# Performance work log

Measured on AMD Instinct MI355X. Metric: run time of the kernel, lower is better.

The kernel has to match this reference:

```python
import jax, jax.numpy as jnp
import numpy as np

D_MODEL = 1024
N_HEADS = 16
HEAD_DIM = D_MODEL // N_HEADS


def setup_inputs() -> dict:
    key = jax.random.key(0)
    ks = jax.random.split(key, 5)
    B, T = 2, 2048
    x = jax.random.normal(ks[0], (B, T, D_MODEL), dtype=jnp.float32)
    s_in = 1.0 / np.sqrt(D_MODEL)
    W_qkv = jax.random.normal(ks[1], (D_MODEL, 3 * D_MODEL), dtype=jnp.float32) * s_in
    b_qkv = jnp.zeros((3 * D_MODEL,), dtype=jnp.float32)
    W_out = jax.random.normal(ks[2], (D_MODEL, D_MODEL), dtype=jnp.float32) * s_in
    b_out = jnp.zeros((D_MODEL,), dtype=jnp.float32)
    gamma = jnp.ones((D_MODEL,), dtype=jnp.float32)
    beta = jnp.zeros((D_MODEL,), dtype=jnp.float32)
    return {"x": x, "W_qkv": W_qkv, "b_qkv": b_qkv, "W_out": W_out,
            "b_out": b_out, "gamma": gamma, "beta": beta}


def _layernorm(x, gamma, beta, eps=1e-5):
    mu = jnp.mean(x, axis=-1, keepdims=True)
    var = jnp.var(x, axis=-1, keepdims=True)
    return (x - mu) * jax.lax.rsqrt(var + eps) * gamma + beta


def reference(x, W_qkv, b_qkv, W_out, b_out, gamma, beta):
    B, T, D = x.shape
    residual = x
    h = _layernorm(x, gamma, beta)
    qkv = h @ W_qkv + b_qkv                      # [B, T, 3D]
    qkv = qkv.reshape(B, T, 3, N_HEADS, HEAD_DIM)
    q = jnp.transpose(qkv[:, :, 0], (0, 2, 1, 3))  # [B, H, T, hd]
    k = jnp.transpose(qkv[:, :, 1], (0, 2, 1, 3))
    v = jnp.transpose(qkv[:, :, 2], (0, 2, 1, 3))
    scale = 1.0 / np.sqrt(HEAD_DIM)
    attn = jnp.einsum("bhqd,bhkd->bhqk", q, k) * scale
    attn = jax.nn.softmax(attn, axis=-1)
    out = jnp.einsum("bhqk,bhkd->bhqd", attn, v)   # [B, H, T, hd]
    out = jnp.transpose(out, (0, 2, 1, 3)).reshape(B, T, D)
    out = out @ W_out + b_out
    return residual + out
```

## Files before the change

kernel.cpp:

```cpp
#include <hip/hip_runtime.h>
#include <hip/hip_bf16.h>


#define DINL static __device__ __forceinline__

typedef __attribute__((ext_vector_type(8))) short bf16x8;
typedef __attribute__((ext_vector_type(4))) float f32x4;

DINL float fast_exp2(float x) { return __builtin_amdgcn_exp2f(x); }

DINL unsigned short f2bf(float f) {
  __hip_bfloat16 h = __float2bfloat16(f);
  unsigned short u;
  __builtin_memcpy(&u, &h, 2);
  return u;
}

DINL unsigned int cvt_pk_bf16(float lo, float hi) {
  unsigned int r;
  asm("v_cvt_pk_bf16_f32 %0, %1, %2" : "=v"(r) : "v"(lo), "v"(hi));
  return r;
}

DINL void gload_lds16(const void* g, void* l) {
  __builtin_amdgcn_global_load_lds((__attribute__((address_space(1))) void*)g,
                                   (__attribute__((address_space(3))) void*)l,
                                   16, 0, 0);
}

__global__ __launch_bounds__(256)
void prep_kernel(const float* __restrict__ x, const float* __restrict__ gamma,
                 const float* __restrict__ beta, unsigned short* __restrict__ h,
                 const float* __restrict__ Wqkv, unsigned short* __restrict__ WqkvT,
                 const float* __restrict__ Wout, unsigned short* __restrict__ WoutT) {
  __shared__ float tile[32][33];
  int bid = blockIdx.x;
  int t = threadIdx.x;

  if (bid < 4096) {
    float* red = &tile[0][0];
    int row = bid;
    float4 v = reinterpret_cast<const float4*>(x + (size_t)row * 1024)[t];
    float s  = v.x + v.y + v.z + v.w;
    float sq = v.x*v.x + v.y*v.y + v.z*v.z + v.w*v.w;
#pragma unroll
    for (int off = 1; off < 64; off <<= 1) {
      s  += __shfl_xor(s, off);
      sq += __shfl_xor(sq, off);
    }
    int wid = t >> 6;
    if ((t & 63) == 0) { red[wid] = s; red[4 + wid] = sq; }
    __syncthreads();
    s  = red[0] + red[1] + red[2] + red[3];
    sq = red[4] + red[5] + red[6] + red[7];
    float mu   = s * (1.0f / 1024.0f);
    float var  = sq * (1.0f / 1024.0f) - mu * mu;
    float rstd = rsqrtf(var + 1e-5f);
    float4 g = reinterpret_cast<const float4*>(gamma)[t];
    float4 b = reinterpret_cast<const float4*>(beta)[t];
    ushort4 o;
    o.x = f2bf((v.x - mu) * rstd * g.x + b.x);
    o.y = f2bf((v.y - mu) * rstd * g.y + b.y);
    o.z = f2bf((v.z - mu) * rstd * g.z + b.z);
    o.w = f2bf((v.w - mu) * rstd * g.w + b.w);
    reinterpret_cast<ushort4*>(h + (size_t)row * 1024)[t] = o;
  } else {
    const float* src;
    unsigned short* dst;
    int R = 1024, C, bx, by;
    if (bid < 7168) {
      src = Wqkv; dst = WqkvT; C = 3072;
      int k = bid - 4096; bx = k % 96; by = k / 96;
    } else {
      src = Wout; dst = WoutT; C = 1024;
      int k = bid - 7168; bx = k & 31; by = k >> 5;
    }
    int tx = t & 31, ty = t >> 5;
    int c0 = bx * 32, r0 = by * 32;
#pragma unroll
    for (int i = 0; i < 4; i++)
      tile[ty + i * 8][tx] = src[(size_t)(r0 + ty + i * 8) * C + c0 + tx];
    __syncthreads();
#pragma unroll
    for (int i = 0; i < 4; i++) {
      int r = ty + i * 8;
      dst[(size_t)(c0 + r) * R + r0 + tx] = f2bf(tile[tx][r]);
    }
  }
}

template <int BM, int MODE, int K>
__global__ __launch_bounds__(256, 4)
void gemm128(const unsigned short* __restrict__ A,
             const unsigned short* __restrict__ Bt,
             const float* __restrict__ bias,
             unsigned short* __restrict__ qdst, unsigned short* __restrict__ kdst,
             unsigned short* __restrict__ vTdst,
             const float* __restrict__ xres, float* __restrict__ out) {
  static_assert(BM == 128 || BM == 64, "");
  constexpr int MR = BM / 32;
  __shared__ unsigned short As[BM * 64];
  __shared__ unsigned short Bs[8192];
  int tid = threadIdx.x, wid = tid >> 6, lane = tid & 63;
  int l15 = lane & 15, l4 = lane >> 4;
  int brow, bcol;
  if (MODE == 0) {
    int lin = blockIdx.y * 24 + blockIdx.x;
    int nl  = (lin & 7) * 96 + (lin >> 3);
    bcol = (nl % 24) * 128;
    brow = (nl / 24) * BM;
  } else {
    brow = blockIdx.y * BM;
    bcol = blockIdx.x * 128;
  }
  int wr = wid >> 1, wc = wid & 1;
  f32x4 acc[MR][4] = {};

  for (int kt = 0; kt < K; kt += 64) {
    __syncthreads();
#pragma unroll
    for (int r = 0; r < MR; r++) {
      int c  = wid * (BM * 2) + r * 64;
      int cl = c + lane;
      int kb = cl / BM, row = cl % BM;
      gload_lds16(A + (size_t)(brow + row) * K + kt + kb * 8, As + c * 8);
    }
#pragma unroll
    for (int r = 0; r < 4; r++) {
      int c  = wid * 256 + r * 64;
      int cl = c + lane;
      int kb = cl >> 7, row = cl & 127;
      gload_lds16(Bt + (size_t)(bcol + row) * K + kt + kb * 8, Bs + c * 8);
    }
    __syncthreads();
#pragma unroll
    for (int ks = 0; ks < 2; ks++) {
      int kb = ks * 4 + l4;
      bf16x8 af[MR], bfr[4];
#pragma unroll
      for (int m = 0; m < MR; m++)
        af[m] = *reinterpret_cast<const bf16x8*>(As + (kb * BM + wr * (BM / 2) + m * 16 + l15) * 8);
#pragma unroll
      for (int n = 0; n < 4; n++)
        bfr[n] = *reinterpret_cast<const bf16x8*>(Bs + (kb * 128 + wc * 64 + n * 16 + l15) * 8);
#pragma unroll
      for (int m = 0; m < MR; m++)
#pragma unroll
        for (int n = 0; n < 4; n++) {
          if (MODE == 0)
            acc[m][n] = __builtin_amdgcn_mfma_f32_16x16x32_bf16(af[m], bfr[n], acc[m][n], 0, 0, 0);
          else
            acc[m][n] = __builtin_amdgcn_mfma_f32_16x16x32_bf16(bfr[n], af[m], acc[m][n], 0, 0, 0);
        }
    }
  }

  if (MODE == 0) {
    int sec = bcol >> 10;
    int secbase = sec << 10;
#pragma unroll
    for (int m = 0; m < MR; m++) {
      int row0 = brow + wr * (BM / 2) + m * 16 + l4 * 4;
      int b = row0 >> 11, t0 = row0 & 2047;
#pragma unroll
      for (int n = 0; n < 4; n++) {
        int col = (bcol & 1023) + wc * 64 + n * 16 + l15;
        float bv = bias[secbase + col];
        int hh = col >> 6, d = col & 63;
        if (sec == 2) {
          ushort4 pk;
          pk.x = f2bf(acc[m][n][0] + bv);
          pk.y = f2bf(acc[m][n][1] + bv);
          pk.z = f2bf(acc[m][n][2] + bv);
          pk.w = f2bf(acc[m][n][3] + bv);
          *reinterpret_cast<ushort4*>(vTdst + ((size_t)(b * 16 + hh) * 64 + d) * 2048 + t0) = pk;
        } else {
          unsigned short* dst = (sec == 0) ? qdst : kdst;
          float sc = (sec == 0) ? 0.125f * 1.44269504088896f : 1.0f;
#pragma unroll
          for (int j = 0; j < 4; j++)
            dst[((size_t)(b * 16 + hh) * 2048 + t0 + j) * 64 + d] = f2bf((acc[m][n][j] + bv) * sc);
        }
      }
    }
  } else {
#pragma unroll
    for (int m = 0; m < MR; m++) {
      int row = brow + wr * (BM / 2) + m * 16 + l15;
#pragma unroll
      for (int n = 0; n < 4; n++) {
        int col0 = bcol + wc * 64 + n * 16 + l4 * 4;
        size_t idx = (size_t)row * 1024 + col0;
        float4 bv = *reinterpret_cast<const float4*>(&bias[col0]);
        float4 xr = *reinterpret_cast<const float4*>(&xres[idx]);
        float4 o;
        o.x = acc[m][n][0] + bv.x + xr.x;
        o.y = acc[m][n][1] + bv.y + xr.y;
        o.z = acc[m][n][2] + bv.z + xr.z;
        o.w = acc[m][n][3] + bv.w + xr.w;
        *reinterpret_cast<float4*>(&out[idx]) = o;
      }
    }
  }
}

__global__ __launch_bounds__(256, 2)
void attn_kernel(const unsigned short* __restrict__ q,
                 const unsigned short* __restrict__ kk,
                 const unsigned short* __restrict__ vT,
                 unsigned short* __restrict__ o) {
  const int T = 2048;
  __shared__ unsigned short Ks[2][8192];
  __shared__ unsigned short Ps[4][2][2048];
  int tid = threadIdx.x, wid = tid >> 6, lane = tid & 63;
  int l15 = lane & 15, l4 = lane >> 4;
  int swz = (l15 & 7) << 3;

  int lin = blockIdx.x;
  int rl  = (lin & 7) * 64 + (lin >> 3);
  int bx = rl & 15, bh = rl >> 4;
  int q0 = bx * 128 + wid * 32;

  const unsigned short* qh = q  + (size_t)bh * T * 64;
  const unsigned short* kh = kk + (size_t)bh * T * 64;
  const unsigned short* vh = vT + (size_t)bh * 64 * T;

  bf16x8 qf[2][2];
#pragma unroll
  for (int m = 0; m < 2; m++)
#pragma unroll
    for (int ks = 0; ks < 2; ks++)
      qf[m][ks] = *reinterpret_cast<const bf16x8*>(
          qh + (size_t)(q0 + m * 16 + l15) * 64 + ks * 32 + l4 * 8);

  f32x4 accO[2][4] = {};
  float lst[2] = {0.0f, 0.0f};

#define STAGE128(buf, kv0)                                                     \
  {                                                                            \
    _Pragma("unroll") for (int r = 0; r < 4; r++) {                            \
      int c  = (wid * 4 + r) * 64;                                             \
      int cl = c + lane;                                                       \
      int key = cl >> 3;                                                       \
      int kb  = (cl & 7) ^ (key & 7);                                          \
      gload_lds16(kh + (size_t)((kv0) + key) * 64 + kb * 8, &Ks[buf][c * 8]);  \
    }                                                                          \
  }

#define QKSM(sub, par)                                                         \
  {                                                                            \
    f32x4 s[2][4] = {};                                                        \
    __builtin_amdgcn_s_setprio(1);                                             \
    _Pragma("unroll") for (int ks = 0; ks < 2; ks++) {                         \
      _Pragma("unroll") for (int n = 0; n < 4; n++) {                          \
        int kkey = (sub) * 64 + n * 16 + l15;                                  \
        int slot = kkey * 8 + ((ks * 4 + l4) ^ (kkey & 7));                    \
        bf16x8 kf = *reinterpret_cast<const bf16x8*>(&Ks[cur][slot * 8]);      \
        _Pragma("unroll") for (int m = 0; m < 2; m++)                          \
          s[m][n] = __builtin_amdgcn_mfma_f32_16x16x32_bf16(kf, qf[m][ks],     \
                                                            s[m][n], 0, 0, 0); \
      }                                                                        \
    }                                                                          \
    __builtin_amdgcn_s_setprio(0);                                             \
    _Pragma("unroll") for (int m = 0; m < 2; m++) {                            \
      float sum = 0.0f;                                                        \
      _Pragma("unroll") for (int n = 0; n < 4; n++) {                          \
        _Pragma("unroll") for (int j = 0; j < 4; j++) {                        \
          float p = fast_exp2(s[m][n][j]);                                     \
          s[m][n][j] = p;                                                      \
          sum += p;                                                            \
        }                                                                      \
        unsigned int u0 = cvt_pk_bf16(s[m][n][0], s[m][n][1]);                 \
        unsigned int u1 = cvt_pk_bf16(s[m][n][2], s[m][n][3]);                 \
        *reinterpret_cast<uint2*>(                                             \
            &Ps[wid][par][(m * 16 + l15) * 64 + ((n * 16 + l4 * 4) ^ swz)]) =  \
            make_uint2(u0, u1);                                                \
      }                                                                        \
      lst[m] += sum;                                                           \
    }                                                                          \
  }

#define PV(par, vf)                                                            \
  {                                                                            \
    __builtin_amdgcn_s_setprio(1);                                             \
    _Pragma("unroll") for (int ks = 0; ks < 2; ks++) {                         \
      _Pragma("unroll") for (int m = 0; m < 2; m++) {                          \
        bf16x8 pf = *reinterpret_cast<const bf16x8*>(                          \
            &Ps[wid][par][(m * 16 + l15) * 64 + ((ks * 32 + l4 * 8) ^ swz)]);  \
        _Pragma("unroll") for (int n = 0; n < 4; n++)                          \
          accO[m][n] = __builtin_amdgcn_mfma_f32_16x16x32_bf16(                \
              vf[ks][n], pf, accO[m][n], 0, 0, 0);                             \
      }                                                                        \
    }                                                                          \
    __builtin_amdgcn_s_setprio(0);                                             \
  }

#define LOADV(vf, kvs)                                                         \
  {                                                                            \
    _Pragma("unroll") for (int ks = 0; ks < 2; ks++)                           \
      _Pragma("unroll") for (int n = 0; n < 4; n++)                            \
        vf[ks][n] = *reinterpret_cast<const bf16x8*>(                          \
            vh + (size_t)(n * 16 + l15) * T + (kvs) + ks * 32 + l4 * 8);       \
  }

  STAGE128(0, 0);
  __syncthreads();
  int cur = 0;

  for (int kv0 = 0; kv0 < T; kv0 += 128) {
    bf16x8 vf0[2][4], vf1[2][4];
    LOADV(vf0, kv0);
    LOADV(vf1, kv0 + 64);
    if (kv0 + 128 < T) STAGE128(cur ^ 1, kv0 + 128);
    QKSM(0, 0);
    QKSM(1, 1);
    PV(0, vf0);
    PV(1, vf1);
    __syncthreads();
    cur ^= 1;
  }
#undef QKSM
#undef PV
#undef LOADV
#undef STAGE128

  int b = bh >> 4, hh = bh & 15;
#pragma unroll
  for (int m = 0; m < 2; m++) {
    float l = lst[m];
    l += __shfl_xor(l, 16);
    l += __shfl_xor(l, 32);
    float inv = 1.0f / l;
    int row = q0 + m * 16 + l15;
#pragma unroll
    for (int n = 0; n < 4; n++) {
      uint2 pk;
      pk.x = cvt_pk_bf16(accO[m][n][0] * inv, accO[m][n][1] * inv);
      pk.y = cvt_pk_bf16(accO[m][n][2] * inv, accO[m][n][3] * inv);
      *reinterpret_cast<uint2*>(
          &o[(size_t)(b * 2048 + row) * 1024 + hh * 64 + n * 16 + l4 * 4]) = pk;
    }
  }
}

extern "C" void kernel_launch(void* const* d_in, const int* in_sizes, int n_in,
                              void* d_out, int out_size, void* d_ws, size_t ws_size,
                              hipStream_t stream) {
  const float* x     = (const float*)d_in[0];
  const float* W_qkv = (const float*)d_in[1];
  const float* b_qkv = (const float*)d_in[2];
  const float* W_out = (const float*)d_in[3];
  const float* b_out = (const float*)d_in[4];
  const float* gamma = (const float*)d_in[5];
  const float* beta  = (const float*)d_in[6];
  float* out = (float*)d_out;

  char* ws = (char*)d_ws;
  const size_t MB = 1024 * 1024;
  unsigned short* h     = (unsigned short*)(ws);
  unsigned short* WqkvT = (unsigned short*)(ws + 8 * MB);
  unsigned short* WoutT = (unsigned short*)(ws + 14 * MB);
  unsigned short* qb    = (unsigned short*)(ws + 16 * MB);
  unsigned short* kb    = (unsigned short*)(ws + 24 * MB);
  unsigned short* vTb   = (unsigned short*)(ws + 32 * MB);
  unsigned short* attno = (unsigned short*)(ws + 40 * MB);

  prep_kernel<<<8192, 256, 0, stream>>>(x, gamma, beta, h, W_qkv, WqkvT, W_out, WoutT);
  gemm128<128, 0, 1024><<<dim3(24, 32), 256, 0, stream>>>(
      h, WqkvT, b_qkv, qb, kb, vTb, nullptr, nullptr);
  attn_kernel<<<512, 256, 0, stream>>>(qb, kb, vTb, attno);
  gemm128<64, 1, 1024><<<dim3(8, 64), 256, 0, stream>>>(
      attno, WoutT, b_out, nullptr, nullptr, nullptr, x, out);
}
```

Measured before the change: 163.1 us.

## Double-buffer LDS in GEMMs and shrink QKV GEMM tile to 64 rows

Replaces the single-buffer GEMM loop with a double-buffered LDS pipeline that issues the next k-tile's global-to-LDS loads before computing on the current tile, with one barrier per iteration. The QKV projection now uses 64-row tiles, which doubles its grid to 1536 blocks, and the XCD swizzle is adjusted to match. Occupancy hint drops to 3 blocks per CU because of the larger LDS footprint. Smaller QKV tiles lower data reuse per block in exchange for more parallelism and overlap of loads with compute.

Result: slower. 182.9 us (+12.1%).

```diff
diff --git a/kernel.cpp b/kernel.cpp
--- a/kernel.cpp
+++ b/kernel.cpp
@@ -89,24 +89,23 @@
   }
 }
 
-template <int BM, int MODE, int K>
-__global__ __launch_bounds__(256, 4)
-void gemm128(const unsigned short* __restrict__ A,
-             const unsigned short* __restrict__ Bt,
-             const float* __restrict__ bias,
-             unsigned short* __restrict__ qdst, unsigned short* __restrict__ kdst,
-             unsigned short* __restrict__ vTdst,
-             const float* __restrict__ xres, float* __restrict__ out) {
-  static_assert(BM == 128 || BM == 64, "");
-  constexpr int MR = BM / 32;
-  __shared__ unsigned short As[BM * 64];
-  __shared__ unsigned short Bs[8192];
+template <int MODE, int K>
+__global__ __launch_bounds__(256, 3)
+void gemm64(const unsigned short* __restrict__ A,
+            const unsigned short* __restrict__ Bt,
+            const float* __restrict__ bias,
+            unsigned short* __restrict__ qdst, unsigned short* __restrict__ kdst,
+            unsigned short* __restrict__ vTdst,
+            const float* __restrict__ xres, float* __restrict__ out) {
+  constexpr int BM = 64;
+  __shared__ unsigned short As[2][4096];
+  __shared__ unsigned short Bs[2][8192];
   int tid = threadIdx.x, wid = tid >> 6, lane = tid & 63;
   int l15 = lane & 15, l4 = lane >> 4;
   int brow, bcol;
   if (MODE == 0) {
     int lin = blockIdx.y * 24 + blockIdx.x;
-    int nl  = (lin & 7) * 96 + (lin >> 3);
+    int nl  = (lin & 7) * 192 + (lin >> 3);
     bcol = (nl % 24) * 128;
     brow = (nl / 24) * BM;
   } else {
@@ -114,37 +113,42 @@
     bcol = blockIdx.x * 128;
   }
   int wr = wid >> 1, wc = wid & 1;
-  f32x4 acc[MR][4] = {};
+  f32x4 acc[2][4] = {};
+
+#define GSTAGE(buf, kt)                                                        \
+  {                                                                            \
+    _Pragma("unroll") for (int r = 0; r < 2; r++) {                            \
+      int c  = wid * 128 + r * 64;                                             \
+      int cl = c + lane;                                                       \
+      int kb = cl >> 6, row = cl & 63;                                         \
+      gload_lds16(A + (size_t)(brow + row) * K + (kt) + kb * 8, As[buf] + c * 8); \
+    }                                                                          \
+    _Pragma("unroll") for (int r = 0; r < 4; r++) {                            \
+      int c  = wid * 256 + r * 64;                                             \
+      int cl = c + lane;                                                       \
+      int kb = cl >> 7, row = cl & 127;                                        \
+      gload_lds16(Bt + (size_t)(bcol + row) * K + (kt) + kb * 8, Bs[buf] + c * 8); \
+    }                                                                          \
+  }
+
+  GSTAGE(0, 0);
+  __syncthreads();
+  int cur = 0;
 
   for (int kt = 0; kt < K; kt += 64) {
-    __syncthreads();
-#pragma unroll
-    for (int r = 0; r < MR; r++) {
-      int c  = wid * (BM * 2) + r * 64;
-      int cl = c + lane;
-      int kb = cl / BM, row = cl % BM;
-      gload_lds16(A + (size_t)(brow + row) * K + kt + kb * 8, As + c * 8);
-    }
-#pragma unroll
-    for (int r = 0; r < 4; r++) {
-      int c  = wid * 256 + r * 64;
-      int cl = c + lane;
-      int kb = cl >> 7, row = cl & 127;
-      gload_lds16(Bt + (size_t)(bcol + row) * K + kt + kb * 8, Bs + c * 8);
-    }
-    __syncthreads();
+    if (kt + 64 < K) GSTAGE(cur ^ 1, kt + 64);
 #pragma unroll
     for (int ks = 0; ks < 2; ks++) {
       int kb = ks * 4 + l4;
-      bf16x8 af[MR], bfr[4];
-#pragma unroll
-      for (int m = 0; m < MR; m++)
-        af[m] = *reinterpret_cast<const bf16x8*>(As + (kb * BM + wr * (BM / 2) + m * 16 + l15) * 8);
+      bf16x8 af[2], bfr[4];
+#pragma unroll
+      for (int m = 0; m < 2; m++)
+        af[m] = *reinterpret_cast<const bf16x8*>(As[cur] + (kb * 64 + wr * 32 + m * 16 + l15) * 8);
 #pragma unroll
       for (int n = 0; n < 4; n++)
-        bfr[n] = *reinterpret_cast<const bf16x8*>(Bs + (kb * 128 + wc * 64 + n * 16 + l15) * 8);
-#pragma unroll
-      for (int m = 0; m < MR; m++)
+        bfr[n] = *reinterpret_cast<const bf16x8*>(Bs[cur] + (kb * 128 + wc * 64 + n * 16 + l15) * 8);
+#pragma unroll
+      for (int m = 0; m < 2; m++)
 #pragma unroll
         for (int n = 0; n < 4; n++) {
           if (MODE == 0)
@@ -153,14 +157,17 @@
             acc[m][n] = __builtin_amdgcn_mfma_f32_16x16x32_bf16(bfr[n], af[m], acc[m][n], 0, 0, 0);
         }
     }
-  }
+    __syncthreads();
+    cur ^= 1;
+  }
+#undef GSTAGE
 
   if (MODE == 0) {
     int sec = bcol >> 10;
     int secbase = sec << 10;
 #pragma unroll
-    for (int m = 0; m < MR; m++) {
-      int row0 = brow + wr * (BM / 2) + m * 16 + l4 * 4;
+    for (int m = 0; m < 2; m++) {
+      int row0 = brow + wr * 32 + m * 16 + l4 * 4;
       int b = row0 >> 11, t0 = row0 & 2047;
 #pragma unroll
       for (int n = 0; n < 4; n++) {
@@ -185,8 +192,8 @@
     }
   } else {
 #pragma unroll
-    for (int m = 0; m < MR; m++) {
-      int row = brow + wr * (BM / 2) + m * 16 + l15;
+    for (int m = 0; m < 2; m++) {
+      int row = brow + wr * 32 + m * 16 + l15;
 #pragma unroll
       for (int n = 0; n < 4; n++) {
         int col0 = bcol + wc * 64 + n * 16 + l4 * 4;
@@ -366,9 +373,9 @@
   unsigned short* attno = (unsigned short*)(ws + 40 * MB);
 
   prep_kernel<<<8192, 256, 0, stream>>>(x, gamma, beta, h, W_qkv, WqkvT, W_out, WoutT);
-  gemm128<128, 0, 1024><<<dim3(24, 32), 256, 0, stream>>>(
+  gemm64<0, 1024><<<dim3(24, 64), 256, 0, stream>>>(
       h, WqkvT, b_qkv, qb, kb, vTb, nullptr, nullptr);
   attn_kernel<<<512, 256, 0, stream>>>(qb, kb, vTb, attno);
-  gemm128<64, 1, 1024><<<dim3(8, 64), 256, 0, stream>>>(
+  gemm64<1, 1024><<<dim3(8, 64), 256, 0, stream>>>(
       attno, WoutT, b_out, nullptr, nullptr, nullptr, x, out);
 }
```

## Widen weight-transpose tiles and store Q transposed for vectorized epilogue writes

Applied to the files above, without the earlier changes.

The weight-transpose path in the prep kernel now uses 64x64 tiles, reading with float4 and writing packed ushort4 rows, so fewer blocks do wider memory transactions. The QKV GEMM epilogue writes Q in a transposed [head][dim][T] layout with 4-wide packed stores, like V, instead of scattered 2-byte stores. In exchange, the attention kernel now gathers its Q fragments with strided scalar loads once per block. The LDS tile read in the transpose (tile[r4*4+k][cc] with row stride 68) may hit bank conflicts.

Result: no change. 165.2 us (+1.3%).

```diff
diff --git a/kernel.cpp b/kernel.cpp
--- a/kernel.cpp
+++ b/kernel.cpp
@@ -33,7 +33,7 @@
                  const float* __restrict__ beta, unsigned short* __restrict__ h,
                  const float* __restrict__ Wqkv, unsigned short* __restrict__ WqkvT,
                  const float* __restrict__ Wout, unsigned short* __restrict__ WoutT) {
-  __shared__ float tile[32][33];
+  __shared__ float tile[64][68];
   int bid = blockIdx.x;
   int t = threadIdx.x;
 
@@ -67,24 +67,33 @@
   } else {
     const float* src;
     unsigned short* dst;
-    int R = 1024, C, bx, by;
-    if (bid < 7168) {
+    int C, bx, by;
+    if (bid < 4864) {
       src = Wqkv; dst = WqkvT; C = 3072;
-      int k = bid - 4096; bx = k % 96; by = k / 96;
+      int k = bid - 4096; bx = k % 48; by = k / 48;
     } else {
       src = Wout; dst = WoutT; C = 1024;
-      int k = bid - 7168; bx = k & 31; by = k >> 5;
-    }
-    int tx = t & 31, ty = t >> 5;
-    int c0 = bx * 32, r0 = by * 32;
-#pragma unroll
-    for (int i = 0; i < 4; i++)
-      tile[ty + i * 8][tx] = src[(size_t)(r0 + ty + i * 8) * C + c0 + tx];
-    __syncthreads();
+      int k = bid - 4864; bx = k & 15; by = k >> 4;
+    }
+    int c0 = bx * 64, r0 = by * 64;
+    int tx = t & 15, ty = t >> 4;
 #pragma unroll
     for (int i = 0; i < 4; i++) {
-      int r = ty + i * 8;
-      dst[(size_t)(c0 + r) * R + r0 + tx] = f2bf(tile[tx][r]);
+      float4 v = *reinterpret_cast<const float4*>(
+          &src[(size_t)(r0 + ty + i * 16) * C + c0 + tx * 4]);
+      *reinterpret_cast<float4*>(&tile[ty + i * 16][tx * 4]) = v;
+    }
+    __syncthreads();
+    int r4 = t & 15, c = t >> 4;
+#pragma unroll
+    for (int i = 0; i < 4; i++) {
+      int cc = c + i * 16;
+      ushort4 pk;
+      pk.x = f2bf(tile[r4 * 4 + 0][cc]);
+      pk.y = f2bf(tile[r4 * 4 + 1][cc]);
+      pk.z = f2bf(tile[r4 * 4 + 2][cc]);
+      pk.w = f2bf(tile[r4 * 4 + 3][cc]);
+      *reinterpret_cast<ushort4*>(&dst[(size_t)(c0 + cc) * 1024 + r0 + r4 * 4]) = pk;
     }
   }
 }
@@ -167,7 +176,15 @@
         int col = (bcol & 1023) + wc * 64 + n * 16 + l15;
         float bv = bias[secbase + col];
         int hh = col >> 6, d = col & 63;
-        if (sec == 2) {
+        if (sec == 0) {
+          const float sc = 0.125f * 1.44269504088896f;
+          ushort4 pk;
+          pk.x = f2bf((acc[m][n][0] + bv) * sc);
+          pk.y = f2bf((acc[m][n][1] + bv) * sc);
+          pk.z = f2bf((acc[m][n][2] + bv) * sc);
+          pk.w = f2bf((acc[m][n][3] + bv) * sc);
+          *reinterpret_cast<ushort4*>(qdst + ((size_t)(b * 16 + hh) * 64 + d) * 2048 + t0) = pk;
+        } else if (sec == 2) {
           ushort4 pk;
           pk.x = f2bf(acc[m][n][0] + bv);
           pk.y = f2bf(acc[m][n][1] + bv);
@@ -175,11 +192,9 @@
           pk.w = f2bf(acc[m][n][3] + bv);
           *reinterpret_cast<ushort4*>(vTdst + ((size_t)(b * 16 + hh) * 64 + d) * 2048 + t0) = pk;
         } else {
-          unsigned short* dst = (sec == 0) ? qdst : kdst;
-          float sc = (sec == 0) ? 0.125f * 1.44269504088896f : 1.0f;
 #pragma unroll
           for (int j = 0; j < 4; j++)
-            dst[((size_t)(b * 16 + hh) * 2048 + t0 + j) * 64 + d] = f2bf((acc[m][n][j] + bv) * sc);
+            kdst[((size_t)(b * 16 + hh) * 2048 + t0 + j) * 64 + d] = f2bf(acc[m][n][j] + bv);
         }
       }
     }
@@ -205,7 +220,7 @@
 }
 
 __global__ __launch_bounds__(256, 2)
-void attn_kernel(const unsigned short* __restrict__ q,
+void attn_kernel(const unsigned short* __restrict__ qT,
                  const unsigned short* __restrict__ kk,
                  const unsigned short* __restrict__ vT,
                  unsigned short* __restrict__ o) {
@@ -221,7 +236,7 @@
   int bx = rl & 15, bh = rl >> 4;
   int q0 = bx * 128 + wid * 32;
 
-  const unsigned short* qh = q  + (size_t)bh * T * 64;
+  const unsigned short* qh = qT + (size_t)bh * 64 * T;
   const unsigned short* kh = kk + (size_t)bh * T * 64;
   const unsigned short* vh = vT + (size_t)bh * 64 * T;
 
@@ -229,9 +244,12 @@
 #pragma unroll
   for (int m = 0; m < 2; m++)
 #pragma unroll
-    for (int ks = 0; ks < 2; ks++)
-      qf[m][ks] = *reinterpret_cast<const bf16x8*>(
-          qh + (size_t)(q0 + m * 16 + l15) * 64 + ks * 32 + l4 * 8);
+    for (int ks = 0; ks < 2; ks++) {
+      int tq = q0 + m * 16 + l15;
+#pragma unroll
+      for (int i = 0; i < 8; i++)
+        qf[m][ks][i] = (short)qh[(size_t)(ks * 32 + l4 * 8 + i) * T + tq];
+    }
 
   f32x4 accO[2][4] = {};
   float lst[2] = {0.0f, 0.0f};
@@ -360,15 +378,15 @@
   unsigned short* h     = (unsigned short*)(ws);
   unsigned short* WqkvT = (unsigned short*)(ws + 8 * MB);
   unsigned short* WoutT = (unsigned short*)(ws + 14 * MB);
-  unsigned short* qb    = (unsigned short*)(ws + 16 * MB);
+  unsigned short* qTb   = (unsigned short*)(ws + 16 * MB);
   unsigned short* kb    = (unsigned short*)(ws + 24 * MB);
   unsigned short* vTb   = (unsigned short*)(ws + 32 * MB);
   unsigned short* attno = (unsigned short*)(ws + 40 * MB);
 
-  prep_kernel<<<8192, 256, 0, stream>>>(x, gamma, beta, h, W_qkv, WqkvT, W_out, WoutT);
+  prep_kernel<<<5120, 256, 0, stream>>>(x, gamma, beta, h, W_qkv, WqkvT, W_out, WoutT);
   gemm128<128, 0, 1024><<<dim3(24, 32), 256, 0, stream>>>(
-      h, WqkvT, b_qkv, qb, kb, vTb, nullptr, nullptr);
-  attn_kernel<<<512, 256, 0, stream>>>(qb, kb, vTb, attno);
+      h, WqkvT, b_qkv, qTb, kb, vTb, nullptr, nullptr);
+  attn_kernel<<<512, 256, 0, stream>>>(qTb, kb, vTb, attno);
   gemm128<64, 1, 1024><<<dim3(8, 64), 256, 0, stream>>>(
       attno, WoutT, b_out, nullptr, nullptr, nullptr, x, out);
 }
```
